# Optimization experiments

Measured on AMD Instinct MI355X. Metric: run time of the kernel, lower is better.

The kernel has to match this reference:

```python
import jax, jax.numpy as jnp
import numpy as np

B, T, LBL = 256, 1024, 128  # batch, seq_len, label_size (incl. start/end)
NUM = LBL - 2               # real emission labels


def setup_inputs() -> dict:
    key = jax.random.key(0)
    k1, k2, k3, k4 = jax.random.split(key, 4)
    logits = jax.random.normal(k1, (B, T, NUM), jnp.float32)
    labels = jax.random.randint(k2, (B, T), 0, NUM)
    lens = jax.random.randint(k3, (B,), 1, T + 1)  # 1..T inclusive
    transition = jax.random.normal(k4, (LBL, LBL), jnp.float32)
    # CRF.initialize(): nothing may transition INTO start-row source or OUT of end
    transition = transition.at[:, LBL - 1].set(-100.0)
    transition = transition.at[LBL - 2, :].set(-100.0)
    return {"logits": logits, "labels": labels, "lens": lens, "transition": transition}


def reference(logits, labels, lens, transition):
    """CRF negative-free log-likelihood pieces: returns gold_score - norm_score per sequence ([B])."""
    Bb, Tt, num = logits.shape
    L = transition.shape[0]
    start, end = L - 2, L - 1

    # pad_logits: append two -1000 columns for start/end labels -> [B, T, L]
    pads = jnp.full((Bb, Tt, 2), -1000.0, logits.dtype)
    lg = jnp.concatenate([logits, pads], axis=2)

    # ---- gold unary score ----
    mask_t = jnp.arange(Tt)[None, :] < lens[:, None]            # [B, T]
    unary = jnp.take_along_axis(lg, labels[..., None], axis=2)[..., 0]
    unary = jnp.where(mask_t, unary, 0.0).sum(axis=1)

    # ---- gold binary (transition) score ----
    ext = jnp.concatenate(
        [jnp.full((Bb, 1), start, labels.dtype), labels,
         jnp.full((Bb, 1), end, labels.dtype)], axis=1)          # [B, T+2]
    mask_e = jnp.arange(Tt + 2)[None, :] < (lens + 1)[:, None]
    ext = jnp.where(mask_e, ext, end)                            # positions >= len+1 -> end
    trn_scr = transition[ext[:, 1:], ext[:, :-1]]                # [B, T+1] (row=next, col=prev)
    mask_b = jnp.arange(Tt + 1)[None, :] < (lens + 1)[:, None]
    binary = jnp.where(mask_b, trn_scr, 0.0).sum(axis=1)

    gold = unary + binary

    # ---- partition (norm) score via log-sum-exp scan over time ----
    alpha0 = jnp.full((Bb, L), -100.0, lg.dtype).at[:, start].set(0.0)
    lg_t = jnp.transpose(lg, (1, 0, 2))                          # [T, B, L]

    def step(alpha, xs):
        logit, t = xs                                            # logit: [B, L]
        # mat[b, j, i] = logit[b, j] + alpha[b, i] + transition[j, i]
        mat = logit[:, :, None] + alpha[:, None, :] + transition[None]
        alpha_nxt = jax.nn.logsumexp(mat, axis=2)                # [B, L]
        alpha = jnp.where((t < lens)[:, None], alpha_nxt, alpha)
        return alpha, None

    alpha, _ = jax.lax.scan(step, alpha0, (lg_t, jnp.arange(Tt)))
    alpha = alpha + transition[end][None, :]
    norm = jax.nn.logsumexp(alpha, axis=1)                       # [B]

    return gold - norm
```

## Files before the change

kernel.cpp:

```cpp
#include <hip/hip_runtime.h>


typedef _Float16 half_t;
typedef _Float16 h2 __attribute__((ext_vector_type(2)));
typedef _Float16 h8 __attribute__((ext_vector_type(8)));

#define TB  1024
#define NUM 126
#define LBL 128

__device__ __forceinline__ float dot2f(h2 a, h2 b, float c) {
  return __builtin_amdgcn_fdot2(a, b, c, false);
}

template <int U>
__device__ __forceinline__ float dotu(h8 a, h8 e, float c) {
  return dot2f(__builtin_shufflevector(a, a, 2 * U, 2 * U + 1),
               __builtin_shufflevector(e, e, 2 * U, 2 * U + 1), c);
}

template <int CTRL>
__device__ __forceinline__ float dpp_max_step(float x) {
  int xi = __float_as_int(x);
  int yi = __builtin_amdgcn_update_dpp(xi, xi, CTRL, 0xF, 0xF, false);
  return fmaxf(x, __int_as_float(yi));
}

__device__ __forceinline__ float wave_max_tree(float x) {
  x = dpp_max_step<0x111>(x);
  x = dpp_max_step<0x112>(x);
  x = dpp_max_step<0x114>(x);
  x = dpp_max_step<0x118>(x);
  x = dpp_max_step<0x142>(x);
  x = dpp_max_step<0x143>(x);
  return x;
}

__device__ __forceinline__ float wave_max64(float x) {
  return __int_as_float(
      __builtin_amdgcn_readlane(__float_as_int(wave_max_tree(x)), 63));
}

template <int CTRL>
__device__ __forceinline__ float dpp_add_step(float x) {
  int xi = __float_as_int(x);
  int yi = __builtin_amdgcn_update_dpp(xi, xi, CTRL, 0xF, 0xF, false);
  return x + __int_as_float(yi);
}

__device__ __forceinline__ float quad_sum(float x) {
  x = dpp_add_step<0xB1>(x);
  x = dpp_add_step<0x4E>(x);
  return x;
}

__global__ __launch_bounds__(256, 1)
void crf_fwd(const float* __restrict__ logits, const int* __restrict__ labels,
             const int* __restrict__ lens, const float* __restrict__ trans,
             float* __restrict__ out)
{
  const int b   = blockIdx.x;
  const int tid = threadIdx.x;
  const int wid = tid >> 6;
  const int l   = tid & 63;
  const int q   = l & 3;
  const int p   = l >> 2;
  const int r0  = (wid << 5) + (p << 1);
  const int r1  = r0 + 1;
  const float rm0 = (r0 < NUM) ? 1.0f : 0.0f;
  const float rm1 = (r1 < NUM) ? 1.0f : 0.0f;
  const int rre = (r0 < NUM - 1) ? r0 : (NUM - 2);
  const int len = lens[b];

  __shared__ __align__(16) h2    a_sh[2][64];
  __shared__ __align__(16) float maxsh[2][4];
  __shared__ float goldsh[4], Msh[4], psh[4];

  const float* lgbase = logits + (size_t)b * TB * NUM;
  const int*   lab    = labels + (size_t)b * TB;

  h8 E0[4], E1[4];
  {
    const float* t0 = trans + r0 * LBL + q * 32;
    const float* t1 = trans + r1 * LBL + q * 32;
    #pragma unroll
    for (int c = 0; c < 4; ++c) {
      h8 v0, v1;
      #pragma unroll
      for (int e = 0; e < 8; ++e) {
        v0[e] = (half_t)__expf(t0[8 * c + e]);
        v1[e] = (half_t)__expf(t1[8 * c + e]);
      }
      E0[c] = v0; E1[c] = v1;
    }
  }

  float g = 0.f;
  #pragma unroll
  for (int kk = 0; kk < 4; ++kk) {
    int t = tid + 256 * kk;
    if (t < len) {
      int lt = lab[t];
      int lp = (t == 0) ? (LBL - 2) : lab[t - 1];
      g += lgbase[(size_t)t * NUM + lt] + trans[lt * LBL + lp];
    }
  }
  if (tid == 0) g += trans[(LBL - 1) * LBL + lab[len - 1]];
  #pragma unroll
  for (int o = 1; o < 64; o <<= 1) g += __shfl_xor(g, o);
  if (l == 0) goldsh[wid] = g;

  if (tid < 64) {
    h2 ai;
    ai[0] = (half_t)((2 * tid     == LBL - 2) ? 1.0f : 0.0f);
    ai[1] = (half_t)((2 * tid + 1 == LBL - 2) ? 1.0f : 0.0f);
    a_sh[0][tid] = ai;
  }
  if (tid < 8) maxsh[tid >> 2][tid & 3] = 64.0f;
  __syncthreads();

  float2 plg[4];
  #pragma unroll
  for (int d = 0; d < 4; ++d)
    plg[d] = *(const float2*)(lgbase + (size_t)d * NUM + rre);

  int P = 6, Kacc = 0, Kout = 0, par = 0;
  float w0_out = 1.f, w1_out = 1.f;

#define DOT8(acc, av, ev)                                                   \
    acc = dotu<0>(av, ev, acc); acc = dotu<1>(av, ev, acc);                 \
    acc = dotu<2>(av, ev, acc); acc = dotu<3>(av, ev, acc);

#define STEP_BODY(Qv)                                                      \
  {                                                                        \
    const float4 mv = *(const float4*)(&maxsh[par][0]);                    \
    const h8* ap = (const h8*)(&a_sh[par][0]) + q * 4;                     \
    float eL0 = __expf((Qv).x) * rm0;                                      \
    float eL1 = __expf((Qv).y) * rm1;                                      \
    h8 av0 = ap[0], av1 = ap[1], av2 = ap[2], av3 = ap[3];                 \
    float sA = 0.f, sB = 0.f, sC = 0.f, sD = 0.f;                          \
    DOT8(sA, av0, E0[0])  DOT8(sC, av0, E1[0])                             \
    DOT8(sA, av1, E0[1])  DOT8(sC, av1, E1[1])                             \
    DOT8(sB, av2, E0[2])  DOT8(sD, av2, E1[2])                             \
    DOT8(sB, av3, E0[3])  DOT8(sD, av3, E1[3])                             \
    float mm = fmaxf(fmaxf(mv.x, mv.y), fmaxf(mv.z, mv.w));                \
    P = (((__float_as_int(mm) >> 23) & 0xFF) - 127) - P + 6;               \
    float w0 = quad_sum(sA + sB) * eL0;                                    \
    float w1 = quad_sum(sC + sD) * eL1;                                    \
    float sc = __int_as_float((127 - P) << 23);           \
    h2 pk;                                                                 \
    pk[0] = (half_t)(w0 * sc);                                             \
    pk[1] = (half_t)(w1 * sc);                                             \
    if (q == 0) a_sh[par ^ 1][(wid << 4) + p] = pk;                        \
    Kout = Kacc;  Kacc += P;                          \
    float m = wave_max_tree(fmaxf(w0, w1));                                \
    if (l == 63) maxsh[par ^ 1][wid] = m;                                  \
           \
    asm volatile("s_waitcnt lgkmcnt(0)\n\ts_barrier" ::: "memory");        \
    w0_out = w0;  w1_out = w1;  par ^= 1;                                  \
  }

  int t = 0;
  for (; t + 4 <= len; t += 4) {
    int q0 = t + 4, q1 = t + 5, q2 = t + 6, q3 = t + 7;
    q0 = (q0 < TB) ? q0 : (TB - 1);  q1 = (q1 < TB) ? q1 : (TB - 1);
    q2 = (q2 < TB) ? q2 : (TB - 1);  q3 = (q3 < TB) ? q3 : (TB - 1);
    STEP_BODY(plg[0])
    plg[0] = *(const float2*)(lgbase + (size_t)q0 * NUM + rre);
    STEP_BODY(plg[1])
    plg[1] = *(const float2*)(lgbase + (size_t)q1 * NUM + rre);
    STEP_BODY(plg[2])
    plg[2] = *(const float2*)(lgbase + (size_t)q2 * NUM + rre);
    STEP_BODY(plg[3])
    plg[3] = *(const float2*)(lgbase + (size_t)q3 * NUM + rre);
  }
  const int rem = len - t;
  if (rem > 0) STEP_BODY(plg[0])
  if (rem > 1) STEP_BODY(plg[1])
  if (rem > 2) STEP_BODY(plg[2])
#undef STEP_BODY
#undef DOT8

  const float LN2 = 0.6931471805599453f;
  float K = (float)Kout * LN2;
  float v0 = K + __logf(w0_out) + trans[(LBL - 1) * LBL + r0];
  float v1 = K + __logf(w1_out) + trans[(LBL - 1) * LBL + r1];
  if (q != 0) { v0 = -__builtin_inff(); v1 = -__builtin_inff(); }
  float M = wave_max64(fmaxf(v0, v1));
  float pp = __expf(v0 - M) + __expf(v1 - M);
  #pragma unroll
  for (int o = 1; o < 64; o <<= 1) pp += __shfl_xor(pp, o);
  if (l == 0) { Msh[wid] = M; psh[wid] = pp; }
  __syncthreads();
  if (tid == 0) {
    float gT = goldsh[0] + goldsh[1] + goldsh[2] + goldsh[3];
    float Mg = fmaxf(fmaxf(Msh[0], Msh[1]), fmaxf(Msh[2], Msh[3]));
    float pg = psh[0] * __expf(Msh[0] - Mg) + psh[1] * __expf(Msh[1] - Mg)
             + psh[2] * __expf(Msh[2] - Mg) + psh[3] * __expf(Msh[3] - Mg);
    out[b] = gT - (Mg + __logf(pg));
  }
}

extern "C" void kernel_launch(void* const* d_in, const int* in_sizes, int n_in,
                              void* d_out, int out_size, void* d_ws, size_t ws_size,
                              hipStream_t stream) {
  const float* logits = (const float*)d_in[0];
  const int*   labels = (const int*)d_in[1];
  const int*   lens   = (const int*)d_in[2];
  const float* trans  = (const float*)d_in[3];
  float* out = (float*)d_out;
  (void)in_sizes; (void)n_in; (void)out_size; (void)d_ws; (void)ws_size;
  crf_fwd<<<256, 256, 0, stream>>>(logits, labels, lens, trans, out);
}
```

Baseline: 482.1 us.

## Remap CRF scan to 4 rows x 8 column-chunks per lane, compute max locally

Each lane now owns four output rows and one 16-wide column chunk of the previous alpha vector, instead of two rows and a 32-wide quarter. Reductions run over 8 lanes using DPP row-shuffle steps. The per-step scaling exponent is no longer read from a shared max array written by each wave. Every wave now takes a packed-f16 max over its own loaded alpha slice and does a full-wave reduction, which removes the shared max buffer and its extra LDS traffic. The cost is more registers for transition exponents, two logit loads per step instead of one, and a longer wave-wide max reduction on the critical path of every timestep.

```diff
diff --git a/kernel.cpp b/kernel.cpp
--- a/kernel.cpp
+++ b/kernel.cpp
@@ -3,7 +3,6 @@
 
 typedef _Float16 half_t;
 typedef _Float16 h2 __attribute__((ext_vector_type(2)));
-typedef _Float16 h8 __attribute__((ext_vector_type(8)));
 
 #define TB  1024
 #define NUM 126
@@ -13,45 +12,47 @@
   return __builtin_amdgcn_fdot2(a, b, c, false);
 }
 
-template <int U>
-__device__ __forceinline__ float dotu(h8 a, h8 e, float c) {
-  return dot2f(__builtin_shufflevector(a, a, 2 * U, 2 * U + 1),
-               __builtin_shufflevector(e, e, 2 * U, 2 * U + 1), c);
+__device__ __forceinline__ h2 bits_h2(unsigned x) {
+  union { unsigned i; h2 h; } u; u.i = x; return u.h;
+}
+__device__ __forceinline__ unsigned h2_bits(h2 h) {
+  union { unsigned i; h2 h; } u; u.h = h; return u.i;
+}
+
+__device__ __forceinline__ unsigned pkmax(unsigned a, unsigned b) {
+  unsigned r;
+  asm("v_pk_max_f16 %0, %1, %2" : "=v"(r) : "v"(a), "v"(b));
+  return r;
 }
 
 template <int CTRL>
-__device__ __forceinline__ float dpp_max_step(float x) {
+__device__ __forceinline__ float dpp_fadd(float x) {
+  int xi = __float_as_int(x);
+  int yi = __builtin_amdgcn_update_dpp(xi, xi, CTRL, 0xF, 0xF, false);
+  return x + __int_as_float(yi);
+}
+template <int CTRL>
+__device__ __forceinline__ float dpp_fmax(float x) {
   int xi = __float_as_int(x);
   int yi = __builtin_amdgcn_update_dpp(xi, xi, CTRL, 0xF, 0xF, false);
   return fmaxf(x, __int_as_float(yi));
 }
 
-__device__ __forceinline__ float wave_max_tree(float x) {
-  x = dpp_max_step<0x111>(x);
-  x = dpp_max_step<0x112>(x);
-  x = dpp_max_step<0x114>(x);
-  x = dpp_max_step<0x118>(x);
-  x = dpp_max_step<0x142>(x);
-  x = dpp_max_step<0x143>(x);
+__device__ __forceinline__ float colsum8(float x) {
+  x = dpp_fadd<0xB1>(x);
+  x = dpp_fadd<0x4E>(x);
+  x = dpp_fadd<0x128>(x);
   return x;
 }
 
 __device__ __forceinline__ float wave_max64(float x) {
-  return __int_as_float(
-      __builtin_amdgcn_readlane(__float_as_int(wave_max_tree(x)), 63));
-}
-
-template <int CTRL>
-__device__ __forceinline__ float dpp_add_step(float x) {
-  int xi = __float_as_int(x);
-  int yi = __builtin_amdgcn_update_dpp(xi, xi, CTRL, 0xF, 0xF, false);
-  return x + __int_as_float(yi);
-}
-
-__device__ __forceinline__ float quad_sum(float x) {
-  x = dpp_add_step<0xB1>(x);
-  x = dpp_add_step<0x4E>(x);
-  return x;
+  x = dpp_fmax<0x111>(x);
+  x = dpp_fmax<0x112>(x);
+  x = dpp_fmax<0x114>(x);
+  x = dpp_fmax<0x118>(x);
+  x = dpp_fmax<0x142>(x);
+  x = dpp_fmax<0x143>(x);
+  return __int_as_float(__builtin_amdgcn_readlane(__float_as_int(x), 63));
 }
 
 __global__ __launch_bounds__(256, 1)
@@ -63,52 +64,52 @@
   const int tid = threadIdx.x;
   const int wid = tid >> 6;
   const int l   = tid & 63;
-  const int q   = l & 3;
-  const int p   = l >> 2;
-  const int r0  = (wid << 5) + (p << 1);
-  const int r1  = r0 + 1;
-  const float rm0 = (r0 < NUM) ? 1.0f : 0.0f;
-  const float rm1 = (r1 < NUM) ? 1.0f : 0.0f;
-  const int rre = (r0 < NUM - 1) ? r0 : (NUM - 2);
+  const int c   = (l & 3) | ((l & 8) >> 1);
+  const int gl  = ((l >> 2) & 1) | ((l >> 3) & 6);
+  const int g   = (wid << 3) | gl;
+  const int row0 = g << 2;
+  const bool writer = ((l & 11) == 0);
+  const float rm0 = (row0 + 0 < NUM) ? 1.0f : 0.0f;
+  const float rm1 = (row0 + 1 < NUM) ? 1.0f : 0.0f;
+  const float rm2 = (row0 + 2 < NUM) ? 1.0f : 0.0f;
+  const float rm3 = (row0 + 3 < NUM) ? 1.0f : 0.0f;
+  const int clb = (row0 <= NUM - 4) ? row0 : (NUM - 4);
+  const bool sh2 = (clb != row0);
   const int len = lens[b];
 
-  __shared__ __align__(16) h2    a_sh[2][64];
-  __shared__ __align__(16) float maxsh[2][4];
+  __shared__ __align__(16) h2 a_sh[2][64];
   __shared__ float goldsh[4], Msh[4], psh[4];
 
   const float* lgbase = logits + (size_t)b * TB * NUM;
   const int*   lab    = labels + (size_t)b * TB;
 
-  h8 E0[4], E1[4];
-  {
-    const float* t0 = trans + r0 * LBL + q * 32;
-    const float* t1 = trans + r1 * LBL + q * 32;
+  h2 E[4][8];
+  #pragma unroll
+  for (int i = 0; i < 4; ++i) {
+    const float* tr = trans + (row0 + i) * LBL + 16 * c;
     #pragma unroll
-    for (int c = 0; c < 4; ++c) {
-      h8 v0, v1;
-      #pragma unroll
-      for (int e = 0; e < 8; ++e) {
-        v0[e] = (half_t)__expf(t0[8 * c + e]);
-        v1[e] = (half_t)__expf(t1[8 * c + e]);
-      }
-      E0[c] = v0; E1[c] = v1;
+    for (int j = 0; j < 8; ++j) {
+      h2 e;
+      e[0] = (half_t)__expf(tr[2 * j]);
+      e[1] = (half_t)__expf(tr[2 * j + 1]);
+      E[i][j] = e;
     }
   }
 
-  float g = 0.f;
+  float gg = 0.f;
   #pragma unroll
   for (int kk = 0; kk < 4; ++kk) {
     int t = tid + 256 * kk;
     if (t < len) {
       int lt = lab[t];
       int lp = (t == 0) ? (LBL - 2) : lab[t - 1];
-      g += lgbase[(size_t)t * NUM + lt] + trans[lt * LBL + lp];
+      gg += lgbase[(size_t)t * NUM + lt] + trans[lt * LBL + lp];
     }
   }
-  if (tid == 0) g += trans[(LBL - 1) * LBL + lab[len - 1]];
-  #pragma unroll
-  for (int o = 1; o < 64; o <<= 1) g += __shfl_xor(g, o);
-  if (l == 0) goldsh[wid] = g;
+  if (tid == 0) gg += trans[(LBL - 1) * LBL + lab[len - 1]];
+  #pragma unroll
+  for (int o = 1; o < 64; o <<= 1) gg += __shfl_xor(gg, o);
+  if (l == 0) goldsh[wid] = gg;
 
   if (tid < 64) {
     h2 ai;
@@ -116,81 +117,112 @@
     ai[1] = (half_t)((2 * tid + 1 == LBL - 2) ? 1.0f : 0.0f);
     a_sh[0][tid] = ai;
   }
-  if (tid < 8) maxsh[tid >> 2][tid & 3] = 64.0f;
   __syncthreads();
 
-  float2 plg[4];
-  #pragma unroll
-  for (int d = 0; d < 4; ++d)
-    plg[d] = *(const float2*)(lgbase + (size_t)d * NUM + rre);
-
-  int P = 6, Kacc = 0, Kout = 0, par = 0;
-  float w0_out = 1.f, w1_out = 1.f;
-
-#define DOT8(acc, av, ev)                                                   \
-    acc = dotu<0>(av, ev, acc); acc = dotu<1>(av, ev, acc);                 \
-    acc = dotu<2>(av, ev, acc); acc = dotu<3>(av, ev, acc);
-
-#define STEP_BODY(Qv)                                                      \
-  {                                                                        \
-    const float4 mv = *(const float4*)(&maxsh[par][0]);                    \
-    const h8* ap = (const h8*)(&a_sh[par][0]) + q * 4;                     \
-    float eL0 = __expf((Qv).x) * rm0;                                      \
-    float eL1 = __expf((Qv).y) * rm1;                                      \
-    h8 av0 = ap[0], av1 = ap[1], av2 = ap[2], av3 = ap[3];                 \
-    float sA = 0.f, sB = 0.f, sC = 0.f, sD = 0.f;                          \
-    DOT8(sA, av0, E0[0])  DOT8(sC, av0, E1[0])                             \
-    DOT8(sA, av1, E0[1])  DOT8(sC, av1, E1[1])                             \
-    DOT8(sB, av2, E0[2])  DOT8(sD, av2, E1[2])                             \
-    DOT8(sB, av3, E0[3])  DOT8(sD, av3, E1[3])                             \
-    float mm = fmaxf(fmaxf(mv.x, mv.y), fmaxf(mv.z, mv.w));                \
-    P = (((__float_as_int(mm) >> 23) & 0xFF) - 127) - P + 6;               \
-    float w0 = quad_sum(sA + sB) * eL0;                                    \
-    float w1 = quad_sum(sC + sD) * eL1;                                    \
-    float sc = __int_as_float((127 - P) << 23);           \
-    h2 pk;                                                                 \
-    pk[0] = (half_t)(w0 * sc);                                             \
-    pk[1] = (half_t)(w1 * sc);                                             \
-    if (q == 0) a_sh[par ^ 1][(wid << 4) + p] = pk;                        \
-    Kout = Kacc;  Kacc += P;                          \
-    float m = wave_max_tree(fmaxf(w0, w1));                                \
-    if (l == 63) maxsh[par ^ 1][wid] = m;                                  \
-           \
-    asm volatile("s_waitcnt lgkmcnt(0)\n\ts_barrier" ::: "memory");        \
-    w0_out = w0;  w1_out = w1;  par ^= 1;                                  \
-  }
+  float2 pA[4], pB[4];
+  #pragma unroll
+  for (int d = 0; d < 4; ++d) {
+    pA[d] = *(const float2*)(lgbase + (size_t)d * NUM + clb);
+    pB[d] = *(const float2*)(lgbase + (size_t)d * NUM + clb + 2);
+  }
+
+  int   Kacc = 0, Kout = 0, par = 0;
+  float w0_out = 1.f, w1_out = 1.f, w2_out = 1.f, w3_out = 1.f;
+
+  auto step = [&](float2 A, float2 B) __attribute__((always_inline)) {
+    const uint4* ap = (const uint4*)(&a_sh[par][8 * c]);
+    uint4 u0 = ap[0], u1 = ap[1];
+    h2 d0 = bits_h2(u0.x), d1 = bits_h2(u0.y), d2 = bits_h2(u0.z), d3 = bits_h2(u0.w);
+    h2 d4 = bits_h2(u1.x), d5 = bits_h2(u1.y), d6 = bits_h2(u1.z), d7 = bits_h2(u1.w);
+    float f0 = sh2 ? B.x : A.x;
+    float f1 = sh2 ? B.y : A.y;
+    float f2 = B.x, f3 = B.y;
+    float eL0 = __expf(f0) * rm0;
+    float eL1 = __expf(f1) * rm1;
+    float eL2 = __expf(f2) * rm2;
+    float eL3 = __expf(f3) * rm3;
+    unsigned m01 = pkmax(u0.x, u0.y), m23 = pkmax(u0.z, u0.w);
+    unsigned m45 = pkmax(u1.x, u1.y), m67 = pkmax(u1.z, u1.w);
+    unsigned mC  = pkmax(pkmax(m01, m23), pkmax(m45, m67));
+    h2 mh = bits_h2(mC);
+    float fm = fmaxf((float)mh[0], (float)mh[1]);
+    float gm = wave_max64(fm);
+    int   P  = ((__float_as_int(gm) >> 23) & 0xFF) - 127 + 6;
+    float s0a = 0.f, s0b = 0.f, s1a = 0.f, s1b = 0.f;
+    float s2a = 0.f, s2b = 0.f, s3a = 0.f, s3b = 0.f;
+    s0a = dot2f(d0, E[0][0], s0a); s0a = dot2f(d1, E[0][1], s0a);
+    s0a = dot2f(d2, E[0][2], s0a); s0a = dot2f(d3, E[0][3], s0a);
+    s0b = dot2f(d4, E[0][4], s0b); s0b = dot2f(d5, E[0][5], s0b);
+    s0b = dot2f(d6, E[0][6], s0b); s0b = dot2f(d7, E[0][7], s0b);
+    s1a = dot2f(d0, E[1][0], s1a); s1a = dot2f(d1, E[1][1], s1a);
+    s1a = dot2f(d2, E[1][2], s1a); s1a = dot2f(d3, E[1][3], s1a);
+    s1b = dot2f(d4, E[1][4], s1b); s1b = dot2f(d5, E[1][5], s1b);
+    s1b = dot2f(d6, E[1][6], s1b); s1b = dot2f(d7, E[1][7], s1b);
+    s2a = dot2f(d0, E[2][0], s2a); s2a = dot2f(d1, E[2][1], s2a);
+    s2a = dot2f(d2, E[2][2], s2a); s2a = dot2f(d3, E[2][3], s2a);
+    s2b = dot2f(d4, E[2][4], s2b); s2b = dot2f(d5, E[2][5], s2b);
+    s2b = dot2f(d6, E[2][6], s2b); s2b = dot2f(d7, E[2][7], s2b);
+    s3a = dot2f(d0, E[3][0], s3a); s3a = dot2f(d1, E[3][1], s3a);
+    s3a = dot2f(d2, E[3][2], s3a); s3a = dot2f(d3, E[3][3], s3a);
+    s3b = dot2f(d4, E[3][4], s3b); s3b = dot2f(d5, E[3][5], s3b);
+    s3b = dot2f(d6, E[3][6], s3b); s3b = dot2f(d7, E[3][7], s3b);
+    float s0 = colsum8(s0a + s0b);
+    float s1 = colsum8(s1a + s1b);
+    float s2 = colsum8(s2a + s2b);
+    float s3 = colsum8(s3a + s3b);
+    float w0 = s0 * eL0, w1 = s1 * eL1, w2 = s2 * eL2, w3 = s3 * eL3;
+    float sc = __int_as_float((127 - P) << 23);
+    h2 pk0, pk1;
+    pk0[0] = (half_t)(w0 * sc);  pk0[1] = (half_t)(w1 * sc);
+    pk1[0] = (half_t)(w2 * sc);  pk1[1] = (half_t)(w3 * sc);
+    if (writer) {
+      uint2 pk2; pk2.x = h2_bits(pk0); pk2.y = h2_bits(pk1);
+      *(uint2*)(&a_sh[par ^ 1][2 * g]) = pk2;
+    }
+    Kout = Kacc;  Kacc += P;
+    asm volatile("s_waitcnt lgkmcnt(0)\n\ts_barrier" ::: "memory");
+    w0_out = w0; w1_out = w1; w2_out = w2; w3_out = w3;
+    par ^= 1;
+  };
 
   int t = 0;
   for (; t + 4 <= len; t += 4) {
     int q0 = t + 4, q1 = t + 5, q2 = t + 6, q3 = t + 7;
     q0 = (q0 < TB) ? q0 : (TB - 1);  q1 = (q1 < TB) ? q1 : (TB - 1);
     q2 = (q2 < TB) ? q2 : (TB - 1);  q3 = (q3 < TB) ? q3 : (TB - 1);
-    STEP_BODY(plg[0])
-    plg[0] = *(const float2*)(lgbase + (size_t)q0 * NUM + rre);
-    STEP_BODY(plg[1])
-    plg[1] = *(const float2*)(lgbase + (size_t)q1 * NUM + rre);
-    STEP_BODY(plg[2])
-    plg[2] = *(const float2*)(lgbase + (size_t)q2 * NUM + rre);
-    STEP_BODY(plg[3])
-    plg[3] = *(const float2*)(lgbase + (size_t)q3 * NUM + rre);
+    step(pA[0], pB[0]);
+    pA[0] = *(const float2*)(lgbase + (size_t)q0 * NUM + clb);
+    pB[0] = *(const float2*)(lgbase + (size_t)q0 * NUM + clb + 2);
+    step(pA[1], pB[1]);
+    pA[1] = *(const float2*)(lgbase + (size_t)q1 * NUM + clb);
+    pB[1] = *(const float2*)(lgbase + (size_t)q1 * NUM + clb + 2);
+    step(pA[2], pB[2]);
+    pA[2] = *(const float2*)(lgbase + (size_t)q2 * NUM + clb);
+    pB[2] = *(const float2*)(lgbase + (size_t)q2 * NUM + clb + 2);
+    step(pA[3], pB[3]);
+    pA[3] = *(const float2*)(lgbase + (size_t)q3 * NUM + clb);
+    pB[3] = *(const float2*)(lgbase + (size_t)q3 * NUM + clb + 2);
   }
   const int rem = len - t;
-  if (rem > 0) STEP_BODY(plg[0])
-  if (rem > 1) STEP_BODY(plg[1])
-  if (rem > 2) STEP_BODY(plg[2])
-#undef STEP_BODY
-#undef DOT8
+  if (rem > 0) step(pA[0], pB[0]);
+  if (rem > 1) step(pA[1], pB[1]);
+  if (rem > 2) step(pA[2], pB[2]);
 
   const float LN2 = 0.6931471805599453f;
   float K = (float)Kout * LN2;
-  float v0 = K + __logf(w0_out) + trans[(LBL - 1) * LBL + r0];
-  float v1 = K + __logf(w1_out) + trans[(LBL - 1) * LBL + r1];
-  if (q != 0) { v0 = -__builtin_inff(); v1 = -__builtin_inff(); }
-  float M = wave_max64(fmaxf(v0, v1));
-  float pp = __expf(v0 - M) + __expf(v1 - M);
-  #pragma unroll
-  for (int o = 1; o < 64; o <<= 1) pp += __shfl_xor(pp, o);
-  if (l == 0) { Msh[wid] = M; psh[wid] = pp; }
+  float vv0 = K + __logf(w0_out) + trans[(LBL - 1) * LBL + row0 + 0];
+  float vv1 = K + __logf(w1_out) + trans[(LBL - 1) * LBL + row0 + 1];
+  float vv2 = K + __logf(w2_out) + trans[(LBL - 1) * LBL + row0 + 2];
+  float vv3 = K + __logf(w3_out) + trans[(LBL - 1) * LBL + row0 + 3];
+  if (!writer) {
+    vv0 = vv1 = vv2 = vv3 = -__builtin_inff();
+  }
+  float vm = fmaxf(fmaxf(vv0, vv1), fmaxf(vv2, vv3));
+  float M = wave_max64(vm);
+  float p = __expf(vv0 - M) + __expf(vv1 - M) + __expf(vv2 - M) + __expf(vv3 - M);
+  #pragma unroll
+  for (int o = 1; o < 64; o <<= 1) p += __shfl_xor(p, o);
+  if (l == 0) { Msh[wid] = M; psh[wid] = p; }
   __syncthreads();
   if (tid == 0) {
     float gT = goldsh[0] + goldsh[1] + goldsh[2] + goldsh[3];
```

Result: slower. 530.6 us (+10.1%).

## Split each row's dot product across 16 lanes using 1024-thread blocks

Applied to the files above, without the earlier changes.

Moves from 256 to 1024 threads per block. Each pair of labels is now handled by 16 lanes, each doing 4 fdot2 operations, where before 4 lanes each did 16. Cross-lane reductions switch from quad to 16-lane row DPP sums, and the per-step max is shared through a 16-entry LDS ring. The aim is a shorter serial dot-product chain on each timestep's critical path. The cost is a barrier across 16 waves every step, more reduction stages, and redundant ring max work.

```diff
diff --git a/kernel.cpp b/kernel.cpp
--- a/kernel.cpp
+++ b/kernel.cpp
@@ -3,7 +3,6 @@
 
 typedef _Float16 half_t;
 typedef _Float16 h2 __attribute__((ext_vector_type(2)));
-typedef _Float16 h8 __attribute__((ext_vector_type(8)));
 
 #define TB  1024
 #define NUM 126
@@ -12,49 +11,51 @@
 __device__ __forceinline__ float dot2f(h2 a, h2 b, float c) {
   return __builtin_amdgcn_fdot2(a, b, c, false);
 }
-
-template <int U>
-__device__ __forceinline__ float dotu(h8 a, h8 e, float c) {
-  return dot2f(__builtin_shufflevector(a, a, 2 * U, 2 * U + 1),
-               __builtin_shufflevector(e, e, 2 * U, 2 * U + 1), c);
+__device__ __forceinline__ h2 bits_h2(unsigned x) {
+  union { unsigned i; h2 h; } u; u.i = x; return u.h;
+}
+__device__ __forceinline__ unsigned h2_bits(h2 h) {
+  union { unsigned i; h2 h; } u; u.h = h; return u.i;
 }
 
 template <int CTRL>
-__device__ __forceinline__ float dpp_max_step(float x) {
+__device__ __forceinline__ float dpp_fadd(float x) {
+  int xi = __float_as_int(x);
+  int yi = __builtin_amdgcn_update_dpp(xi, xi, CTRL, 0xF, 0xF, false);
+  return x + __int_as_float(yi);
+}
+template <int CTRL>
+__device__ __forceinline__ float dpp_fmax(float x) {
   int xi = __float_as_int(x);
   int yi = __builtin_amdgcn_update_dpp(xi, xi, CTRL, 0xF, 0xF, false);
   return fmaxf(x, __int_as_float(yi));
 }
 
-__device__ __forceinline__ float wave_max_tree(float x) {
-  x = dpp_max_step<0x111>(x);
-  x = dpp_max_step<0x112>(x);
-  x = dpp_max_step<0x114>(x);
-  x = dpp_max_step<0x118>(x);
-  x = dpp_max_step<0x142>(x);
-  x = dpp_max_step<0x143>(x);
+__device__ __forceinline__ float rowsum16(float x) {
+  x = dpp_fadd<0x121>(x);
+  x = dpp_fadd<0x122>(x);
+  x = dpp_fadd<0x124>(x);
+  x = dpp_fadd<0x128>(x);
   return x;
 }
-
+__device__ __forceinline__ float rowmax16(float x) {
+  x = dpp_fmax<0x121>(x);
+  x = dpp_fmax<0x122>(x);
+  x = dpp_fmax<0x124>(x);
+  x = dpp_fmax<0x128>(x);
+  return x;
+}
 __device__ __forceinline__ float wave_max64(float x) {
-  return __int_as_float(
-      __builtin_amdgcn_readlane(__float_as_int(wave_max_tree(x)), 63));
-}
-
-template <int CTRL>
-__device__ __forceinline__ float dpp_add_step(float x) {
-  int xi = __float_as_int(x);
-  int yi = __builtin_amdgcn_update_dpp(xi, xi, CTRL, 0xF, 0xF, false);
-  return x + __int_as_float(yi);
-}
-
-__device__ __forceinline__ float quad_sum(float x) {
-  x = dpp_add_step<0xB1>(x);
-  x = dpp_add_step<0x4E>(x);
-  return x;
-}
-
-__global__ __launch_bounds__(256, 1)
+  x = dpp_fmax<0x111>(x);
+  x = dpp_fmax<0x112>(x);
+  x = dpp_fmax<0x114>(x);
+  x = dpp_fmax<0x118>(x);
+  x = dpp_fmax<0x142>(x);
+  x = dpp_fmax<0x143>(x);
+  return __int_as_float(__builtin_amdgcn_readlane(__float_as_int(x), 63));
+}
+
+__global__ __launch_bounds__(1024, 1)
 void crf_fwd(const float* __restrict__ logits, const int* __restrict__ labels,
              const int* __restrict__ lens, const float* __restrict__ trans,
              float* __restrict__ out)
@@ -63,52 +64,48 @@
   const int tid = threadIdx.x;
   const int wid = tid >> 6;
   const int l   = tid & 63;
-  const int q   = l & 3;
-  const int p   = l >> 2;
-  const int r0  = (wid << 5) + (p << 1);
-  const int r1  = r0 + 1;
+  const int c   = l & 15;
+  const int g   = (wid << 2) | (l >> 4);
+  const int r0  = 2 * g;
+  const int r1  = 2 * g + 1;
   const float rm0 = (r0 < NUM) ? 1.0f : 0.0f;
   const float rm1 = (r1 < NUM) ? 1.0f : 0.0f;
-  const int rre = (r0 < NUM - 1) ? r0 : (NUM - 2);
+  const int clb = (r0 < NUM - 1) ? r0 : (NUM - 2);
   const int len = lens[b];
 
   __shared__ __align__(16) h2    a_sh[2][64];
-  __shared__ __align__(16) float maxsh[2][4];
-  __shared__ float goldsh[4], Msh[4], psh[4];
+  __shared__ __align__(16) float ring[2][16];
+  __shared__ float goldsh[16], Msh[16], psh[16];
 
   const float* lgbase = logits + (size_t)b * TB * NUM;
   const int*   lab    = labels + (size_t)b * TB;
 
-  h8 E0[4], E1[4];
+  h2 E0[4], E1[4];
   {
-    const float* t0 = trans + r0 * LBL + q * 32;
-    const float* t1 = trans + r1 * LBL + q * 32;
-    #pragma unroll
-    for (int c = 0; c < 4; ++c) {
-      h8 v0, v1;
-      #pragma unroll
-      for (int e = 0; e < 8; ++e) {
-        v0[e] = (half_t)__expf(t0[8 * c + e]);
-        v1[e] = (half_t)__expf(t1[8 * c + e]);
-      }
-      E0[c] = v0; E1[c] = v1;
+    const float* t0 = trans + r0 * LBL + 8 * c;
+    const float* t1 = trans + r1 * LBL + 8 * c;
+    #pragma unroll
+    for (int k = 0; k < 4; ++k) {
+      h2 e0, e1;
+      e0[0] = (half_t)__expf(t0[2 * k]);  e0[1] = (half_t)__expf(t0[2 * k + 1]);
+      e1[0] = (half_t)__expf(t1[2 * k]);  e1[1] = (half_t)__expf(t1[2 * k + 1]);
+      E0[k] = e0;  E1[k] = e1;
     }
   }
 
-  float g = 0.f;
-  #pragma unroll
-  for (int kk = 0; kk < 4; ++kk) {
-    int t = tid + 256 * kk;
+  float gacc = 0.f;
+  {
+    int t = tid;
     if (t < len) {
       int lt = lab[t];
       int lp = (t == 0) ? (LBL - 2) : lab[t - 1];
-      g += lgbase[(size_t)t * NUM + lt] + trans[lt * LBL + lp];
+      gacc = lgbase[(size_t)t * NUM + lt] + trans[lt * LBL + lp];
     }
-  }
-  if (tid == 0) g += trans[(LBL - 1) * LBL + lab[len - 1]];
-  #pragma unroll
-  for (int o = 1; o < 64; o <<= 1) g += __shfl_xor(g, o);
-  if (l == 0) goldsh[wid] = g;
+    if (tid == 0) gacc += trans[(LBL - 1) * LBL + lab[len - 1]];
+    #pragma unroll
+    for (int o = 1; o < 64; o <<= 1) gacc += __shfl_xor(gacc, o);
+    if (l == 0) goldsh[wid] = gacc;
+  }
 
   if (tid < 64) {
     h2 ai;
@@ -116,87 +113,83 @@
     ai[1] = (half_t)((2 * tid + 1 == LBL - 2) ? 1.0f : 0.0f);
     a_sh[0][tid] = ai;
   }
-  if (tid < 8) maxsh[tid >> 2][tid & 3] = 64.0f;
+  if (tid < 32) ring[tid >> 4][tid & 15] = 64.0f;
   __syncthreads();
 
   float2 plg[4];
   #pragma unroll
   for (int d = 0; d < 4; ++d)
-    plg[d] = *(const float2*)(lgbase + (size_t)d * NUM + rre);
-
-  int P = 6, Kacc = 0, Kout = 0, par = 0;
+    plg[d] = *(const float2*)(lgbase + (size_t)d * NUM + clb);
+
+  int   P = 6, Kacc = 0, Kout = 0, par = 0;
   float w0_out = 1.f, w1_out = 1.f;
 
-#define DOT8(acc, av, ev)                                                   \
-    acc = dotu<0>(av, ev, acc); acc = dotu<1>(av, ev, acc);                 \
-    acc = dotu<2>(av, ev, acc); acc = dotu<3>(av, ev, acc);
-
-#define STEP_BODY(Qv)                                                      \
-  {                                                                        \
-    const float4 mv = *(const float4*)(&maxsh[par][0]);                    \
-    const h8* ap = (const h8*)(&a_sh[par][0]) + q * 4;                     \
-    float eL0 = __expf((Qv).x) * rm0;                                      \
-    float eL1 = __expf((Qv).y) * rm1;                                      \
-    h8 av0 = ap[0], av1 = ap[1], av2 = ap[2], av3 = ap[3];                 \
-    float sA = 0.f, sB = 0.f, sC = 0.f, sD = 0.f;                          \
-    DOT8(sA, av0, E0[0])  DOT8(sC, av0, E1[0])                             \
-    DOT8(sA, av1, E0[1])  DOT8(sC, av1, E1[1])                             \
-    DOT8(sB, av2, E0[2])  DOT8(sD, av2, E1[2])                             \
-    DOT8(sB, av3, E0[3])  DOT8(sD, av3, E1[3])                             \
-    float mm = fmaxf(fmaxf(mv.x, mv.y), fmaxf(mv.z, mv.w));                \
-    P = (((__float_as_int(mm) >> 23) & 0xFF) - 127) - P + 6;               \
-    float w0 = quad_sum(sA + sB) * eL0;                                    \
-    float w1 = quad_sum(sC + sD) * eL1;                                    \
-    float sc = __int_as_float((127 - P) << 23);           \
-    h2 pk;                                                                 \
-    pk[0] = (half_t)(w0 * sc);                                             \
-    pk[1] = (half_t)(w1 * sc);                                             \
-    if (q == 0) a_sh[par ^ 1][(wid << 4) + p] = pk;                        \
-    Kout = Kacc;  Kacc += P;                          \
-    float m = wave_max_tree(fmaxf(w0, w1));                                \
-    if (l == 63) maxsh[par ^ 1][wid] = m;                                  \
-           \
-    asm volatile("s_waitcnt lgkmcnt(0)\n\ts_barrier" ::: "memory");        \
-    w0_out = w0;  w1_out = w1;  par ^= 1;                                  \
-  }
+  auto step = [&](float2 Qv) __attribute__((always_inline)) {
+    float rv = ring[par][c];
+    const uint4 av = *(const uint4*)((const unsigned*)&a_sh[par][0] + 4 * c);
+    h2 d0 = bits_h2(av.x), d1 = bits_h2(av.y), d2 = bits_h2(av.z), d3 = bits_h2(av.w);
+    float eL0 = __expf(Qv.x) * rm0;
+    float eL1 = __expf(Qv.y) * rm1;
+    float s0 = 0.f, s1 = 0.f;
+    s0 = dot2f(d0, E0[0], s0);  s1 = dot2f(d0, E1[0], s1);
+    s0 = dot2f(d1, E0[1], s0);  s1 = dot2f(d1, E1[1], s1);
+    s0 = dot2f(d2, E0[2], s0);  s1 = dot2f(d2, E1[2], s1);
+    s0 = dot2f(d3, E0[3], s0);  s1 = dot2f(d3, E1[3], s1);
+    float rmax = rowmax16(rv);
+    P = (((__float_as_int(rmax) >> 23) & 0xFF) - 127) - P + 6;
+    float w0 = rowsum16(s0) * eL0;
+    float w1 = rowsum16(s1) * eL1;
+    float sc = __int_as_float((127 - P) << 23);
+    h2 pk;
+    pk[0] = (half_t)(w0 * sc);
+    pk[1] = (half_t)(w1 * sc);
+    if (c == 0) a_sh[par ^ 1][g] = pk;
+    Kout = Kacc;  Kacc += P;
+    float wm = fmaxf(w0, w1);
+    wm = dpp_fmax<0x142>(wm);
+    wm = dpp_fmax<0x143>(wm);
+    if (l == 63) ring[par ^ 1][wid] = wm;
+    asm volatile("s_waitcnt lgkmcnt(0)\n\ts_barrier" ::: "memory");
+    w0_out = w0;  w1_out = w1;  par ^= 1;
+  };
 
   int t = 0;
   for (; t + 4 <= len; t += 4) {
     int q0 = t + 4, q1 = t + 5, q2 = t + 6, q3 = t + 7;
     q0 = (q0 < TB) ? q0 : (TB - 1);  q1 = (q1 < TB) ? q1 : (TB - 1);
     q2 = (q2 < TB) ? q2 : (TB - 1);  q3 = (q3 < TB) ? q3 : (TB - 1);
-    STEP_BODY(plg[0])
-    plg[0] = *(const float2*)(lgbase + (size_t)q0 * NUM + rre);
-    STEP_BODY(plg[1])
-    plg[1] = *(const float2*)(lgbase + (size_t)q1 * NUM + rre);
-    STEP_BODY(plg[2])
-    plg[2] = *(const float2*)(lgbase + (size_t)q2 * NUM + rre);
-    STEP_BODY(plg[3])
-    plg[3] = *(const float2*)(lgbase + (size_t)q3 * NUM + rre);
+    step(plg[0]);
+    plg[0] = *(const float2*)(lgbase + (size_t)q0 * NUM + clb);
+    step(plg[1]);
+    plg[1] = *(const float2*)(lgbase + (size_t)q1 * NUM + clb);
+    step(plg[2]);
+    plg[2] = *(const float2*)(lgbase + (size_t)q2 * NUM + clb);
+    step(plg[3]);
+    plg[3] = *(const float2*)(lgbase + (size_t)q3 * NUM + clb);
   }
   const int rem = len - t;
-  if (rem > 0) STEP_BODY(plg[0])
-  if (rem > 1) STEP_BODY(plg[1])
-  if (rem > 2) STEP_BODY(plg[2])
-#undef STEP_BODY
-#undef DOT8
+  if (rem > 0) step(plg[0]);
+  if (rem > 1) step(plg[1]);
+  if (rem > 2) step(plg[2]);
 
   const float LN2 = 0.6931471805599453f;
   float K = (float)Kout * LN2;
   float v0 = K + __logf(w0_out) + trans[(LBL - 1) * LBL + r0];
   float v1 = K + __logf(w1_out) + trans[(LBL - 1) * LBL + r1];
-  if (q != 0) { v0 = -__builtin_inff(); v1 = -__builtin_inff(); }
+  if (c != 0) { v0 = -__builtin_inff(); v1 = -__builtin_inff(); }
   float M = wave_max64(fmaxf(v0, v1));
-  float pp = __expf(v0 - M) + __expf(v1 - M);
+  float p = __expf(v0 - M) + __expf(v1 - M);
   #pragma unroll
-  for (int o = 1; o < 64; o <<= 1) pp += __shfl_xor(pp, o);
-  if (l == 0) { Msh[wid] = M; psh[wid] = pp; }
+  for (int o = 1; o < 64; o <<= 1) p += __shfl_xor(p, o);
+  if (l == 0) { Msh[wid] = M; psh[wid] = p; }
   __syncthreads();
   if (tid == 0) {
-    float gT = goldsh[0] + goldsh[1] + goldsh[2] + goldsh[3];
-    float Mg = fmaxf(fmaxf(Msh[0], Msh[1]), fmaxf(Msh[2], Msh[3]));
-    float pg = psh[0] * __expf(Msh[0] - Mg) + psh[1] * __expf(Msh[1] - Mg)
-             + psh[2] * __expf(Msh[2] - Mg) + psh[3] * __expf(Msh[3] - Mg);
+    float gT = 0.f, Mg = -__builtin_inff();
+    #pragma unroll
+    for (int i = 0; i < 16; ++i) { gT += goldsh[i]; Mg = fmaxf(Mg, Msh[i]); }
+    float pg = 0.f;
+    #pragma unroll
+    for (int i = 0; i < 16; ++i) pg += psh[i] * __expf(Msh[i] - Mg);
     out[b] = gT - (Mg + __logf(pg));
   }
 }
@@ -210,5 +203,5 @@
   const float* trans  = (const float*)d_in[3];
   float* out = (float*)d_out;
   (void)in_sizes; (void)n_in; (void)out_size; (void)d_ws; (void)ws_size;
-  crf_fwd<<<256, 256, 0, stream>>>(logits, labels, lens, trans, out);
-}
+  crf_fwd<<<256, 1024, 0, stream>>>(logits, labels, lens, trans, out);
+}
```

After: 759.0 us. +57.4%, slower.
